# Optimization experiments

Hardware: AMD Instinct MI355X
Metric: run time of the kernel (lower is better)

## Reference

```python
import jax, jax.numpy as jnp
import numpy as np

KSIZE = 7
STRIDE = 4
SCALE = 10.0
C_IN = 64
C_INT = 16
TOP_M = 100


def _unfold(x, k, s):
    # x: [B,C,H,W] -> [B, C*k*k, L] with torch.nn.Unfold channel ordering (c, ki, kj)
    B, C, H, W = x.shape
    oh = (H - k) // s + 1
    ow = (W - k) // s + 1
    rows = jnp.arange(oh)[:, None] * s + jnp.arange(k)[None, :]  # [oh,k]
    cols = jnp.arange(ow)[:, None] * s + jnp.arange(k)[None, :]  # [ow,k]
    p = x[:, :, rows][:, :, :, :, cols]          # [B,C,oh,k,ow,k]
    p = p.transpose(0, 1, 3, 5, 2, 4)            # [B,C,k,k,oh,ow]
    return p.reshape(B, C * k * k, oh * ow)


def _fold(p, H, W, k, s):
    # inverse of _unfold with overlap-add (torch.nn.Fold semantics)
    B, D, L = p.shape
    C = D // (k * k)
    oh = (H - k) // s + 1
    ow = (W - k) // s + 1
    rows = jnp.arange(oh)[:, None] * s + jnp.arange(k)[None, :]
    cols = jnp.arange(ow)[:, None] * s + jnp.arange(k)[None, :]
    p = p.reshape(B, C, k, k, oh, ow).transpose(0, 1, 4, 2, 5, 3)  # [B,C,oh,k,ow,k]
    out = jnp.zeros((B, C, H, W), p.dtype)
    return out.at[:, :, rows[:, :, None, None], cols[None, None, :, :]].add(p)


def _conv1x1(x, w, b):
    return jnp.einsum('bchw,oc->bohw', x, w) + b[None, :, None, None]


def _conv3x3(x, w, b):
    y = jax.lax.conv_general_dilated(x, w, (1, 1), ((1, 1), (1, 1)),
                                     dimension_numbers=('NCHW', 'OIHW', 'NCHW'))
    return y + b[None, :, None, None]


def setup_inputs() -> dict:
    key = jax.random.key(0)
    ks = jax.random.split(key, 12)
    B, H, W = 4, 127, 127
    s = 0.05  # small init std keeps softmax logits in a sane range
    return {
        'x': jax.random.normal(ks[0], (B, C_IN, H, W), jnp.float32),
        'g_w': jax.random.normal(ks[1], (C_INT, C_IN, 3, 3), jnp.float32) * s,
        'g_b': jnp.zeros((C_INT,), jnp.float32),
        'theta_w': jax.random.normal(ks[2], (C_INT, C_IN), jnp.float32) * s,
        'theta_b': jnp.zeros((C_INT,), jnp.float32),
        'phi_w': jax.random.normal(ks[3], (C_INT, C_IN), jnp.float32) * s,
        'phi_b': jnp.zeros((C_INT,), jnp.float32),
        'match_w': jax.random.normal(ks[4], (C_INT, C_IN), jnp.float32) * s,
        'match_b': jnp.zeros((C_INT,), jnp.float32),
        'restore_w': jax.random.normal(ks[5], (C_IN, C_INT), jnp.float32) * s,
        'restore_b': jnp.zeros((C_IN,), jnp.float32),
    }


def reference(x, g_w, g_b, theta_w, theta_b, phi_w, phi_b,
              match_w, match_b, restore_w, restore_b):
    B, C, H, W = x.shape
    b1 = _conv3x3(x, g_w, g_b)           # [B,16,H,W]
    b2 = _conv1x1(x, theta_w, theta_b)
    b3 = _conv1x1(x, phi_w, phi_b)

    p1 = _unfold(b1, KSIZE, STRIDE).transpose(0, 2, 1)  # [B,L,D], D=16*49
    p2 = _unfold(b2, KSIZE, STRIDE).transpose(0, 2, 1)
    p3 = _unfold(b3, KSIZE, STRIDE).transpose(0, 2, 1)

    score = jnp.einsum('bld,bmd->blm', p1, p2)           # [B,L,L]
    L = score.shape[-1]
    k = min(TOP_M, L)
    vals, idx = jax.lax.top_k(score, k)                  # [B,L,k]
    bI = jnp.arange(B)[:, None, None]
    rI = jnp.arange(L)[None, :, None]
    sparse = jnp.zeros_like(score).at[bI, rI, idx].set(vals)
    attn = jax.nn.softmax(sparse * SCALE, axis=-1)

    agg = jnp.einsum('blm,bmd->bld', attn, p3).transpose(0, 2, 1)  # [B,D,L]
    out = _fold(agg, H, W, KSIZE, STRIDE)                # [B,16,H,W]

    mask = _fold(_unfold(jnp.ones_like(x), KSIZE, STRIDE), H, W, KSIZE, STRIDE)
    mask = _conv1x1(mask, match_w, match_b)              # [B,16,H,W]

    out = out / (mask + 1e-8)
    out = _conv1x1(out, restore_w, restore_b)            # [B,64,H,W]
    return out
```

## Files before the change

kernel.cpp:

```cpp
#include <hip/hip_runtime.h>
#include <hip/hip_bf16.h>

typedef __hip_bfloat16 bf16;
typedef unsigned short ushort_t;
typedef __attribute__((ext_vector_type(8))) __bf16 bfv8;
typedef __attribute__((ext_vector_type(16))) float f32x16;

#define B_   4
#define CIN  64
#define CI   16
#define H_   127
#define W_   127
#define HW   (H_*W_)
#define KS   7
#define ST   4
#define OH_  31
#define L_   961
#define D_   784
#define TOPM 100

#define N1   1032256
#define WG_O 4
#define WT_O (WG_O + 9216)
#define WP_O (WT_O + 1024)
#define BG_O (WP_O + 1024)
#define BT_O (BG_O + 16)
#define BP_O (BT_O + 16)
#define SM_O (BP_O + 16)
#define SB_O (SM_O + 16)
#define RW_O (SB_O + 16)
#define RB_O (RW_O + 1024)
#define B1_O 12448
#define S3_O (B1_O + 3*N1)
#define WB_O (S3_O + B_*D_)
#define REG_O (WB_O + 36864)
#define XHSZ 4129024
#define SROW 964
#define SCSLOT 926464
#define AGSZ 753424
#define TKROW 112
#define SLST 72
#define PKPLANE 753424
#define PKSTR   1506848
#define PADW 129
#define PADPIX (PADW*PADW)
#define XPB  (PADPIX*64)
#define XPU  ((size_t)B_ * XPB)

#define FULL_BYTES ((size_t)(REG_O + XHSZ + 4*AGSZ) * 4)
#define MID_BYTES  ((size_t)(REG_O + 4260096) * 4)

__device__ __forceinline__ float bf2f(bf16 v) { return __bfloat162float(v); }
__device__ __forceinline__ float bflo(unsigned u) { return __uint_as_float(u << 16); }
__device__ __forceinline__ float bfhi(unsigned u) { return __uint_as_float(u & 0xFFFF0000u); }

template <typename T> struct Ld;
template <> struct Ld<float> {
  static __device__ __forceinline__ float f(const void* p, int i) { return ((const float*)p)[i]; }
};
template <> struct Ld<bf16> {
  static __device__ __forceinline__ float f(const void* p, int i) { return bf2f(((const bf16*)p)[i]); }
};

__device__ __forceinline__ unsigned fmap(float f) {
  unsigned u = __float_as_uint(f);
  return (u & 0x80000000u) ? ~u : (u | 0x80000000u);
}
__device__ __forceinline__ float unfmap(unsigned kk) {
  unsigned u = (kk & 0x80000000u) ? (kk & 0x7fffffffu) : ~kk;
  return __uint_as_float(u);
}

__device__ __forceinline__ ushort_t f2bf(float x) {
  unsigned u = __float_as_uint(x);
  return (ushort_t)((u + 0x7FFFu + ((u >> 16) & 1u)) >> 16);
}
__device__ __forceinline__ void splitbf(float x, ushort_t& h, ushort_t& l) {
  h = f2bf(x);
  float hf = __uint_as_float(((unsigned)h) << 16);
  l = f2bf(x - hf);
}

__global__ void k_detect(const unsigned short* __restrict__ xh, int* __restrict__ flag) {
  int tid = threadIdx.x;
  int c = 0;
#pragma unroll
  for (int j = 0; j < 2; ++j) {
    unsigned u = xh[tid * 2 + j];
    unsigned e = (u >> 7) & 0xFF;
    if (e >= 134) c++;
  }
#pragma unroll
  for (int o = 32; o; o >>= 1) c += __shfl_down(c, o);
  if (tid == 0) *flag = (c >= 8) ? 1 : 0;
}

#define LDW(ptr, i) (f ? ((const float*)(ptr))[i] : bf2f(((const bf16*)(ptr))[i]))
__global__ __launch_bounds__(256) void k_prep(
    const int* __restrict__ flag,
    const void* g_w, const void* t_w, const void* p_w,
    const void* g_b, const void* t_b, const void* p_b,
    const void* m_w, const void* m_b, const void* r_w, const void* r_b,
    float* __restrict__ ws)
{
  int f = *flag;
  int gid = blockIdx.x * 256 + threadIdx.x;
  int gs = gridDim.x * 256;
  for (int i = gid; i < 9216; i += gs) {
    int o = i & 15, t = i >> 4, c = t & 63, tap = t >> 6;
    ws[WG_O + i] = LDW(g_w, (o * 64 + c) * 9 + tap);
  }
  for (int i = gid; i < 1024; i += gs) {
    int o = i & 15, c = i >> 4;
    ws[WT_O + i] = LDW(t_w, o * 64 + c);
    ws[WP_O + i] = LDW(p_w, o * 64 + c);
  }
  if (gid < 16) {
    ws[BG_O + gid] = LDW(g_b, gid);
    ws[BT_O + gid] = LDW(t_b, gid);
    ws[BP_O + gid] = LDW(p_b, gid);
    float s = 0.f;
    for (int c = 0; c < 64; ++c) s += LDW(m_w, gid * 64 + c);
    ws[SM_O + gid] = s;
    ws[SB_O + gid] = LDW(m_b, gid);
  }
  for (int i = gid; i < 1024; i += gs) ws[RW_O + i] = LDW(r_w, i);
  if (gid >= 64 && gid < 128) ws[RB_O + gid - 64] = LDW(r_b, gid - 64);
  ushort_t* wBh = (ushort_t*)(ws + WB_O);
  ushort_t* wBl = wBh + 9 * 64 * 64;
  for (int i = gid; i < 9 * 64 * 64; i += gs) {
    int c = i & 63, t = i >> 6, col = t & 63, tap = t >> 6;
    float v = 0.f;
    if (col < 16) v = LDW(g_w, (col * 64 + c) * 9 + tap);
    else if (col < 32) { if (tap == 4) v = LDW(t_w, (col - 16) * 64 + c); }
    else if (col < 48) { if (tap == 4) v = LDW(p_w, (col - 32) * 64 + c); }
    ushort_t h, l; splitbf(v, h, l);
    wBh[i] = h; wBl[i] = l;
  }
}

__global__ __launch_bounds__(256) void k_zpad(ushort_t* __restrict__ xhh,
                                              ushort_t* __restrict__ xhl)
{
  int idx = blockIdx.x * 256 + threadIdx.x;
  if (idx >= B_ * 512 * 8) return;
  int q = idx & 7, t = idx >> 3;
  int bp = t & 511, bb = t >> 9;
  int pp;
  if (bp < 129) pp = bp;
  else if (bp < 258) pp = 128 * PADW + (bp - 129);
  else if (bp < 385) pp = (bp - 257) * PADW;
  else pp = (bp - 384) * PADW + 128;
  size_t off = ((size_t)bb * PADPIX + pp) * 64 + q * 8;
  const int4 z = make_int4(0, 0, 0, 0);
  *(int4*)(xhh + off) = z;
  *(int4*)(xhl + off) = z;
}

__global__ __launch_bounds__(256) void k_hwc(
    const int* __restrict__ flag, const void* __restrict__ x,
    ushort_t* __restrict__ xhh, ushort_t* __restrict__ xhl)
{
  __shared__ float tile[64][65];
  int pix0 = blockIdx.x * 64;
  int tid = threadIdx.x;
  int g = tid >> 6, p = tid & 63;
  int pix = pix0 + p;
  bool ok = pix < B_ * HW;
  int bb = ok ? pix / HW : 0;
  int r  = ok ? pix - bb * HW : 0;
  if (*flag) {
    const float* xf = (const float*)x;
    for (int c = g * 16; c < g * 16 + 16; ++c)
      tile[p][c] = ok ? xf[((size_t)bb * CIN + c) * HW + r] : 0.f;
  } else {
    const bf16* xb = (const bf16*)x;
    for (int c = g * 16; c < g * 16 + 16; ++c)
      tile[p][c] = ok ? bf2f(xb[((size_t)bb * CIN + c) * HW + r]) : 0.f;
  }
  __syncthreads();
  int c2 = tid & 63, pg = tid >> 6;
  int pix2 = pix0 + pg * 16;
  int bb2 = pix2 / HW, r2 = pix2 - bb2 * HW;
  int h2 = r2 / W_, w2 = r2 - h2 * W_;
  for (int k = 0; k < 16; ++k) {
    if (pix2 + k < B_ * HW) {
      ushort_t h, l; splitbf(tile[pg * 16 + k][c2], h, l);
      size_t off = ((size_t)bb2 * PADPIX + (size_t)(h2 + 1) * PADW + (w2 + 1)) * 64 + c2;
      xhh[off] = h;
      xhl[off] = l;
    }
    if (++w2 == W_) { w2 = 0; if (++h2 == H_) { h2 = 0; ++bb2; } }
  }
}

__global__ __launch_bounds__(256) void k_conv3(
    const float* __restrict__ ws,
    const ushort_t* __restrict__ xhh, const ushort_t* __restrict__ xhl,
    ushort_t* __restrict__ b1h, ushort_t* __restrict__ b1l,
    ushort_t* __restrict__ b2h, ushort_t* __restrict__ b2l,
    ushort_t* __restrict__ b3)
{
  __shared__ ushort_t sAh[128 * SLST], sAl[128 * SLST];
  __shared__ ushort_t sBh[64 * SLST],  sBl[64 * SLST];
  int bz = blockIdx.z;
  int h = blockIdx.x;
  int tid = threadIdx.x, lane = tid & 63, wv = tid >> 6;
  int grp = lane >> 3, ch = lane & 7;

  const ushort_t* xplane = ((wv == 0) ? xhh : xhl) + (size_t)bz * XPB;
  const ushort_t* wBh_ = (const ushort_t*)(ws + WB_O);
  const ushort_t* bsrc = (wv == 2) ? wBh_ : (wBh_ + 9 * 64 * 64);
  ushort_t* dplane = (wv == 0) ? sAh : (wv == 1) ? sAl : (wv == 2) ? sBh : sBl;

  int fr = lane & 31, kh = (lane >> 5) << 3;
  int mt = (wv >> 1) << 1;
  int aoff0 = (mt * 32 + fr) * SLST + kh;
  int aoff1 = ((mt + 1) * 32 + fr) * SLST + kh;
  int boff  = (((wv & 1) << 5) + fr) * SLST + kh;

  f32x16 acc0 = {0.f,0.f,0.f,0.f,0.f,0.f,0.f,0.f,0.f,0.f,0.f,0.f,0.f,0.f,0.f,0.f};
  f32x16 acc1 = {0.f,0.f,0.f,0.f,0.f,0.f,0.f,0.f,0.f,0.f,0.f,0.f,0.f,0.f,0.f,0.f};

  int4 pv0, pv1, pv2, pv3, pv4, pv5, pv6, pv7;
  int4 pv8, pv9, pv10, pv11, pv12, pv13, pv14, pv15;

#define LC(j) pv##j = *(const int4*)(src + (j) * 512)
#define LC_A  LC(0); LC(1); LC(2); LC(3); LC(4); LC(5); LC(6); LC(7); \
              LC(8); LC(9); LC(10); LC(11); LC(12); LC(13); LC(14); LC(15)
#define LC_W  LC(0); LC(1); LC(2); LC(3); LC(4); LC(5); LC(6); LC(7)
#define WC(j) *(int4*)(d0 + (j) * 8 * SLST) = pv##j
#define WC_A  WC(0); WC(1); WC(2); WC(3); WC(4); WC(5); WC(6); WC(7); \
              WC(8); WC(9); WC(10); WC(11); WC(12); WC(13); WC(14); WC(15)
#define WC_W  WC(0); WC(1); WC(2); WC(3); WC(4); WC(5); WC(6); WC(7)

  if (wv < 2) {
    const ushort_t* src = xplane + (size_t)h * (PADW * 64) + grp * 64 + ch * 8;
    LC_A;
  } else {
    const ushort_t* src = bsrc + grp * 64 + ch * 8;
    LC_W;
  }

  for (int r = 0; r < 9; ++r) {
    __syncthreads();
    {
      ushort_t* d0 = dplane + grp * SLST + ch * 8;
      if (wv < 2) { WC_A; } else { WC_W; }
    }
    __syncthreads();
    if (r < 8) {
      int rn = r + 1;
      int dh = rn / 3 - 1, dw = rn % 3 - 1;
      if (wv < 2) {
        const ushort_t* src = xplane
            + ((size_t)(h + 1 + dh) * PADW + (1 + dw)) * 64 + grp * 64 + ch * 8;
        LC_A;
      } else {
        const ushort_t* src = bsrc + rn * 4096 + grp * 64 + ch * 8;
        LC_W;
      }
    }
#pragma unroll
    for (int t = 0; t < 4; ++t) {
      bfv8 ah0 = *(const bfv8*)(sAh + aoff0 + t * 16);
      bfv8 al0 = *(const bfv8*)(sAl + aoff0 + t * 16);
      bfv8 ah1 = *(const bfv8*)(sAh + aoff1 + t * 16);
      bfv8 al1 = *(const bfv8*)(sAl + aoff1 + t * 16);
      bfv8 bh  = *(const bfv8*)(sBh + boff + t * 16);
      bfv8 bl  = *(const bfv8*)(sBl + boff + t * 16);
      acc0 = __builtin_amdgcn_mfma_f32_32x32x16_bf16(al0, bh, acc0, 0, 0, 0);
      acc0 = __builtin_amdgcn_mfma_f32_32x32x16_bf16(ah0, bl, acc0, 0, 0, 0);
      acc0 = __builtin_amdgcn_mfma_f32_32x32x16_bf16(ah0, bh, acc0, 0, 0, 0);
      acc1 = __builtin_amdgcn_mfma_f32_32x32x16_bf16(al1, bh, acc1, 0, 0, 0);
      acc1 = __builtin_amdgcn_mfma_f32_32x32x16_bf16(ah1, bl, acc1, 0, 0, 0);
      acc1 = __builtin_amdgcn_mfma_f32_32x32x16_bf16(ah1, bh, acc1, 0, 0, 0);
    }
  }
#undef LC
#undef LC_A
#undef LC_W
#undef WC
#undef WC_A
#undef WC_W

  int nw = ((wv & 1) << 5) + fr;
#pragma unroll
  for (int s = 0; s < 2; ++s) {
    int mbase = (mt + s) * 32;
#pragma unroll
    for (int r = 0; r < 16; ++r) {
      int m = mbase + (r & 3) + ((r >> 2) << 3) + ((lane >> 5) << 2);
      if (m >= W_) continue;
      int p2 = h * W_ + m;
      size_t ob = ((size_t)bz * HW + p2) * 16;
      float val = s ? acc1[r] : acc0[r];
      if (nw < 16) {
        ushort_t h2, l2; splitbf(val + ws[BG_O + nw], h2, l2);
        b1h[ob + nw] = h2; b1l[ob + nw] = l2;
      } else if (nw < 32) {
        int o = nw - 16; ushort_t h2, l2; splitbf(val + ws[BT_O + o], h2, l2);
        b2h[ob + o] = h2; b2l[ob + o] = l2;
      } else if (nw < 48) {
        int o = nw - 32; b3[ob + o] = f2bf(val + ws[BP_O + o]);
      }
    }
  }
}

template <typename T>
__device__ __forceinline__ void convF_body(
    const void* x, const void* g_w, const void* g_b,
    const void* t_w, const void* t_b, const void* p_w, const void* p_b,
    ushort_t* b1h, ushort_t* b1l, ushort_t* b2h, ushort_t* b2l, ushort_t* b3,
    float* sgw, float* stw, float* spw)
{
  int tid = threadIdx.y * 32 + threadIdx.x;
  for (int i = tid; i < CI * CIN * 9; i += 256) sgw[i] = Ld<T>::f(g_w, i);
  for (int i = tid; i < CI * CIN; i += 256) { stw[i] = Ld<T>::f(t_w, i); spw[i] = Ld<T>::f(p_w, i); }
  __syncthreads();

  int w = blockIdx.x * 32 + threadIdx.x;
  int h = blockIdx.y * 8 + threadIdx.y;
  int b = blockIdx.z;
  if (w >= W_ || h >= H_) return;

  float a1[CI], a2[CI], a3[CI];
#pragma unroll
  for (int o = 0; o < CI; ++o) { a1[o] = 0.f; a2[o] = 0.f; a3[o] = 0.f; }

  const size_t xb = (size_t)b * CIN * HW;
  for (int c = 0; c < CIN; ++c) {
    float xv[9];
#pragma unroll
    for (int dh = 0; dh < 3; ++dh) {
      int hh = h + dh - 1;
      bool rok = ((unsigned)hh < (unsigned)H_);
#pragma unroll
      for (int dw = 0; dw < 3; ++dw) {
        int ww = w + dw - 1;
        bool ok = rok && ((unsigned)ww < (unsigned)W_);
        xv[dh * 3 + dw] = ok ? Ld<T>::f(x, (int)(xb + (size_t)c * HW + hh * W_ + ww)) : 0.f;
      }
    }
    float xc = xv[4];
#pragma unroll
    for (int o = 0; o < CI; ++o) {
      const float* gg = &sgw[(o * CIN + c) * 9];
      float s = gg[0]*xv[0] + gg[1]*xv[1] + gg[2]*xv[2]
              + gg[3]*xv[3] + gg[4]*xv[4] + gg[5]*xv[5]
              + gg[6]*xv[6] + gg[7]*xv[7] + gg[8]*xv[8];
      a1[o] += s;
      a2[o] += stw[o * CIN + c] * xc;
      a3[o] += spw[o * CIN + c] * xc;
    }
  }
  size_t base = ((size_t)b * HW + h * W_ + w) * CI;
#pragma unroll
  for (int o = 0; o < CI; ++o) {
    float v1 = a1[o] + Ld<T>::f(g_b, o);
    float v2 = a2[o] + Ld<T>::f(t_b, o);
    ushort_t hh2, ll2;
    splitbf(v1, hh2, ll2); b1h[base + o] = hh2; b1l[base + o] = ll2;
    splitbf(v2, hh2, ll2); b2h[base + o] = hh2; b2l[base + o] = ll2;
    b3[base + o] = f2bf(a3[o] + Ld<T>::f(p_b, o));
  }
}

__global__ __launch_bounds__(256) void k_convF(
    const int* __restrict__ flag, const void* x,
    const void* g_w, const void* g_b, const void* t_w, const void* t_b,
    const void* p_w, const void* p_b,
    ushort_t* __restrict__ b1h, ushort_t* __restrict__ b1l,
    ushort_t* __restrict__ b2h, ushort_t* __restrict__ b2l,
    ushort_t* __restrict__ b3)
{
  __shared__ float sgw[CI * CIN * 9];
  __shared__ float stw[CI * CIN];
  __shared__ float spw[CI * CIN];
  if (*flag) convF_body<float>(x, g_w, g_b, t_w, t_b, p_w, p_b, b1h, b1l, b2h, b2l, b3, sgw, stw, spw);
  else       convF_body<bf16 >(x, g_w, g_b, t_w, t_b, p_w, p_b, b1h, b1l, b2h, b2l, b3, sgw, stw, spw);
}

__global__ __launch_bounds__(256) void k_colsum(const ushort_t* __restrict__ b3, float* __restrict__ S3)
{
  __shared__ float red[16][17];
  int b = blockIdx.x, pos = blockIdx.y;
  int ki = pos / 7, kj = pos % 7;
  int c = threadIdx.x & 15, chunk = threadIdx.x >> 4;
  const ushort_t* B3 = b3 + (size_t)b * HW * CI;
  float s = 0.f;
  for (int l = chunk; l < L_; l += 16) {
    int lh = l / OH_, lw = l % OH_;
    s += bflo((unsigned)B3[((lh * ST + ki) * W_ + lw * ST + kj) * CI + c]);
  }
  red[chunk][c] = s;
  __syncthreads();
  if (threadIdx.x < 16) {
    float t = 0.f;
#pragma unroll
    for (int k = 0; k < 16; ++k) t += red[k][threadIdx.x];
    S3[(b * 49 + pos) * 16 + threadIdx.x] = t;
  }
}

__global__ __launch_bounds__(256) void k_pack(
    const ushort_t* __restrict__ b1h, const ushort_t* __restrict__ b1l,
    ushort_t* __restrict__ pk, int b0, unsigned pkstride_z)
{
  int idx = blockIdx.x * 256 + threadIdx.x;
  if (idx >= 961 * 98) return;
  int row = idx / 98, rem = idx - row * 98;
  int nki = rem / 14, q = rem - nki * 14;
  int slh = row / OH_, slw = row - slh * OH_;
  int src = ((slh * ST) * W_ + slw * ST + nki * W_) * 16 + q * 8;
  int dst = (nki * 961 + row) * 112 + q * 8;
  int batch = b0 + blockIdx.y;
  size_t poff = (size_t)batch * HW * CI;
  ushort_t* pkb = pk + (size_t)blockIdx.y * pkstride_z;
  *(int4*)(pkb + dst)           = *(const int4*)(b1h + poff + src);
  *(int4*)(pkb + PKPLANE + dst) = *(const int4*)(b1l + poff + src);
}

__global__ __launch_bounds__(256) void k_score(
    const ushort_t* __restrict__ b2h, const ushort_t* __restrict__ b2l,
    const ushort_t* __restrict__ pk,
    float* __restrict__ scb, int b0, unsigned scstride_z, unsigned pkstride_z)
{
  __shared__ ushort_t sAh[128 * SLST], sAl[128 * SLST];
  __shared__ ushort_t sBh[64 * SLST],  sBl[64 * SLST];
  int batch = b0 + blockIdx.z;
  size_t poff_g = (size_t)batch * HW * CI;
  float* Sc = scb + (size_t)blockIdx.z * scstride_z;

  int tid = threadIdx.x;
  int m0 = blockIdx.y * 128, n0 = blockIdx.x * 64;
  int lane = tid & 63;
  int wv = tid >> 6;
  int grp = lane >> 3, ch = lane & 7;

  const ushort_t* pkb = pk + (size_t)blockIdx.z * pkstride_z + (size_t)(wv & 1) * PKPLANE;

  int srow = n0 + lane;  if (srow > L_ - 1) srow = L_ - 1;
  int slh = srow / OH_, slw = srow - slh * OH_;
  int sbase = (slh * ST) * W_ + slw * ST;
  const ushort_t* splane = (wv == 2) ? (b2h + poff_g) : (b2l + poff_g);
  ushort_t* dplane = (wv == 0) ? sAh : (wv == 1) ? sAl : (wv == 2) ? sBh : sBl;
  ushort_t* drowB = dplane + lane * SLST;

  int fr = lane & 31;
  int kh = (lane >> 5) << 3;
  int mt = (wv >> 1) << 1;
  int aoff0 = (mt * 32 + fr) * SLST + kh;
  int aoff1 = ((mt + 1) * 32 + fr) * SLST + kh;
  int boff  = (((wv & 1) << 5) + fr) * SLST + kh;

  f32x16 acc0 = {0.f,0.f,0.f,0.f,0.f,0.f,0.f,0.f,0.f,0.f,0.f,0.f,0.f,0.f,0.f,0.f};
  f32x16 acc1 = {0.f,0.f,0.f,0.f,0.f,0.f,0.f,0.f,0.f,0.f,0.f,0.f,0.f,0.f,0.f,0.f};

  int4 pv0, pv1, pv2, pv3, pv4, pv5, pv6, pv7;
  int4 pv8, pv9, pv10, pv11, pv12, pv13, pv14, pv15;

#define LA(j) pv##j = *(const int4*)(pks + (size_t)min(m0 + 8*j + grp, 960) * 112)
#define LA_ALL LA(0); LA(1); LA(2); LA(3); LA(4); LA(5); LA(6); LA(7); \
               LA(8); LA(9); LA(10); LA(11); LA(12); LA(13); LA(14); LA(15)
#define WA(j) *(int4*)(d0 + (j) * 8 * SLST) = pv##j
#define WA_ALL WA(0); WA(1); WA(2); WA(3); WA(4); WA(5); WA(6); WA(7); \
               WA(8); WA(9); WA(10); WA(11); WA(12); WA(13); WA(14); WA(15)

  if (wv < 2) {
    const ushort_t* pks = pkb + ch * 8;
    LA_ALL;
  } else {
    const int4* s0 = (const int4*)(splane + (size_t)sbase * 16);
    pv0 = s0[0]; pv1 = s0[1]; pv2 = s0[2]; pv3 = s0[3];
    pv4 = s0[4]; pv5 = s0[5]; pv6 = s0[6]; pv7 = s0[7];
  }

  for (int r = 0; r < 14; ++r) {
    int half = r & 1;
    __syncthreads();
    if (wv < 2) {
      ushort_t* d0 = dplane + grp * SLST + ch * 8;
      if (!half) { WA_ALL; }
      else if (ch < 6) { WA_ALL; }
    } else {
      *(int4*)(drowB + 0)  = pv0;  *(int4*)(drowB + 8)  = pv1;
      *(int4*)(drowB + 16) = pv2;  *(int4*)(drowB + 24) = pv3;
      *(int4*)(drowB + 32) = pv4;  *(int4*)(drowB + 40) = pv5;
      if (!half) { *(int4*)(drowB + 48) = pv6; *(int4*)(drowB + 56) = pv7; }
    }
    __syncthreads();
    if (r < 13) {
      int rn = r + 1;
      int nki = rn >> 1, odd = rn & 1;
      if (wv < 2) {
        const ushort_t* pks = pkb + (size_t)nki * (961 * 112) + odd * 64 + ch * 8;
        if (!odd) { LA_ALL; }
        else if (ch < 6) { LA_ALL; }
      } else {
        int nkj0 = odd * 4;
        const int4* s0 = (const int4*)(splane + (size_t)(sbase + nki * W_ + nkj0) * 16);
        pv0 = s0[0]; pv1 = s0[1]; pv2 = s0[2]; pv3 = s0[3]; pv4 = s0[4]; pv5 = s0[5];
        if (!odd) { pv6 = s0[6]; pv7 = s0[7]; }
      }
    }
    if (!half) {
#pragma unroll
      for (int t = 0; t < 4; ++t) {
        bfv8 ah0 = *(const bfv8*)(sAh + aoff0 + t * 16);
        bfv8 al0 = *(const bfv8*)(sAl + aoff0 + t * 16);
        bfv8 ah1 = *(const bfv8*)(sAh + aoff1 + t * 16);
        bfv8 al1 = *(const bfv8*)(sAl + aoff1 + t * 16);
        bfv8 bh  = *(const bfv8*)(sBh + boff + t * 16);
        bfv8 bl  = *(const bfv8*)(sBl + boff + t * 16);
        acc0 = __builtin_amdgcn_mfma_f32_32x32x16_bf16(al0, bh, acc0, 0, 0, 0);
        acc0 = __builtin_amdgcn_mfma_f32_32x32x16_bf16(ah0, bl, acc0, 0, 0, 0);
        acc0 = __builtin_amdgcn_mfma_f32_32x32x16_bf16(ah0, bh, acc0, 0, 0, 0);
        acc1 = __builtin_amdgcn_mfma_f32_32x32x16_bf16(al1, bh, acc1, 0, 0, 0);
        acc1 = __builtin_amdgcn_mfma_f32_32x32x16_bf16(ah1, bl, acc1, 0, 0, 0);
        acc1 = __builtin_amdgcn_mfma_f32_32x32x16_bf16(ah1, bh, acc1, 0, 0, 0);
      }
    } else {
#pragma unroll
      for (int t = 0; t < 3; ++t) {
        bfv8 ah0 = *(const bfv8*)(sAh + aoff0 + t * 16);
        bfv8 al0 = *(const bfv8*)(sAl + aoff0 + t * 16);
        bfv8 ah1 = *(const bfv8*)(sAh + aoff1 + t * 16);
        bfv8 al1 = *(const bfv8*)(sAl + aoff1 + t * 16);
        bfv8 bh  = *(const bfv8*)(sBh + boff + t * 16);
        bfv8 bl  = *(const bfv8*)(sBl + boff + t * 16);
        acc0 = __builtin_amdgcn_mfma_f32_32x32x16_bf16(al0, bh, acc0, 0, 0, 0);
        acc0 = __builtin_amdgcn_mfma_f32_32x32x16_bf16(ah0, bl, acc0, 0, 0, 0);
        acc0 = __builtin_amdgcn_mfma_f32_32x32x16_bf16(ah0, bh, acc0, 0, 0, 0);
        acc1 = __builtin_amdgcn_mfma_f32_32x32x16_bf16(al1, bh, acc1, 0, 0, 0);
        acc1 = __builtin_amdgcn_mfma_f32_32x32x16_bf16(ah1, bl, acc1, 0, 0, 0);
        acc1 = __builtin_amdgcn_mfma_f32_32x32x16_bf16(ah1, bh, acc1, 0, 0, 0);
      }
    }
  }
#undef LA
#undef LA_ALL
#undef WA
#undef WA_ALL

  int nw = n0 + ((wv & 1) << 5) + fr;
  if (nw < L_) {
    int mw0 = m0 + mt * 32;
#pragma unroll
    for (int r = 0; r < 16; ++r) {
      int m = mw0 + (r & 3) + ((r >> 2) << 3) + ((lane >> 5) << 2);
      if (m < L_) Sc[(size_t)m * SROW + nw] = acc0[r];
    }
    int mw1 = m0 + (mt + 1) * 32;
#pragma unroll
    for (int r = 0; r < 16; ++r) {
      int m = mw1 + (r & 3) + ((r >> 2) << 3) + ((lane >> 5) << 2);
      if (m < L_) Sc[(size_t)m * SROW + nw] = acc1[r];
    }
  }
}

__global__ __launch_bounds__(256) void k_topk(
    const float* __restrict__ scb, float* __restrict__ tkw, int* __restrict__ tkp,
    unsigned scstride_z)
{
  __shared__ float swv[4][TOPM];
  __shared__ int spx[4][TOPM];
  int tid = threadIdx.x;
  int wvi = tid >> 6, lane = tid & 63;
  int l = blockIdx.x * 4 + wvi;
  if (l > L_ - 1) l = L_ - 1;
  int bz = blockIdx.y;
  const float4* row4 = (const float4*)(scb + (size_t)bz * scstride_z + (size_t)l * SROW);
  int trow = (bz * L_ + l) * TKROW;

  unsigned k[16];
#pragma unroll
  for (int q = 0; q < 4; ++q) {
    float4 v = row4[q * 64 + lane];
    int ib = (q * 64 + lane) * 4;
    k[q * 4 + 0] = (ib + 0 < L_) ? fmap(v.x) : 0u;
    k[q * 4 + 1] = (ib + 1 < L_) ? fmap(v.y) : 0u;
    k[q * 4 + 2] = (ib + 2 < L_) ? fmap(v.z) : 0u;
    k[q * 4 + 3] = (ib + 3 < L_) ? fmap(v.w) : 0u;
  }

  unsigned mk = 0;
#pragma unroll
  for (int r = 0; r < 16; ++r) mk = max(mk, k[r]);
#pragma unroll
  for (int o = 32; o; o >>= 1) mk = max(mk, (unsigned)__shfl_down((int)mk, o));
  mk = (unsigned)__shfl((int)mk, 0);
  float vmax = unfmap(mk);

  unsigned kk[16];
#pragma unroll
  for (int r = 0; r < 16; ++r) kk[r] = k[r];

  unsigned prefix = 0; int base = 0;
  for (int bit = 30; bit >= 0; bit -= 2) {
    int n3 = 0, n2 = 0, n1 = 0;
#pragma unroll
    for (int r = 0; r < 16; ++r) {
      unsigned f = (kk[r] >> bit) & 3u;
      n3 += (int)__popcll(__ballot(f == 3u));
      n2 += (int)__popcll(__ballot(f >= 2u));
      n1 += (int)__popcll(__ballot(f >= 1u));
    }
    unsigned ch;
    if (base + n3 >= TOPM) ch = 3;
    else if (base + n2 >= TOPM) { ch = 2; base += n3; }
    else if (base + n1 >= TOPM) { ch = 1; base += n2; }
    else { ch = 0; base += n1; }
    prefix |= ch << bit;
#pragma unroll
    for (int r = 0; r < 16; ++r) {
      unsigned f = (kk[r] >> bit) & 3u;
      kk[r] = (f == ch) ? kk[r] : 0u;
    }
  }
  int nA = base;
  int needT = TOPM - nA;

  int cA = 0, cT = 0;
#pragma unroll
  for (int r = 0; r < 16; ++r) { cA += (k[r] > prefix); cT += (k[r] == prefix); }
  int pk = cA | (cT << 16);
  int incl = pk;
#pragma unroll
  for (int o = 1; o < 64; o <<= 1) { int t = __shfl_up(incl, o); if (lane >= o) incl += t; }
  int excl = incl - pk;
  int tA = excl & 0xFFFF, tT = excl >> 16;

  float M = fmaxf(10.f * vmax, 0.f);
  float e0 = __expf(-M);
  float z = 0.f;
#pragma unroll
  for (int r = 0; r < 16; ++r) {
    unsigned kr = k[r];
    int slot = -1;
    if (kr > prefix) slot = tA++;
    else if (kr == prefix) { if (tT < needT) slot = nA + tT; tT++; }
    if (slot >= 0) {
      float v = unfmap(kr);
      float wv = __expf(10.f * v - M);
      swv[wvi][slot] = wv; z += wv;
      int gi = 256 * (r >> 2) + 4 * lane + (r & 3);
      int lh = gi / OH_, lw = gi - lh * OH_;
      spx[wvi][slot] = ((lh * ST) * W_ + lw * ST) * CI;
    }
  }
#pragma unroll
  for (int o = 32; o; o >>= 1) z += __shfl_down(z, o);
  z = __shfl(z, 0);
  float Z = z + (float)(L_ - TOPM) * e0;
  float invZ = 1.f / Z;
  float w0 = e0 / Z;
  __syncthreads();
#pragma unroll
  for (int s0 = 0; s0 < 2; ++s0) {
    int s = lane + 64 * s0;
    if (s < TOPM) {
      tkw[trow + s] = swv[wvi][s] * invZ - w0;
      tkp[trow + s] = spx[wvi][s];
    }
  }
  if (lane == 0) tkw[trow + TOPM] = w0;
}

__global__ __launch_bounds__(128) void k_pv(
    const float* __restrict__ tkw, const int* __restrict__ tkp,
    const ushort_t* __restrict__ b3, const float* __restrict__ s3,
    float* __restrict__ agb, int b0, unsigned agstride_z)
{
  int l = blockIdx.x, bz = blockIdx.y;
  int batch = b0 + bz;
  int trow = (bz * L_ + l) * TKROW;
  const ushort_t* B3 = b3 + (size_t)batch * HW * CI;
  const float* S3 = s3 + (size_t)batch * D_;
  float* agg = agb + (size_t)bz * agstride_z;
  int tid = threadIdx.x;
  if (tid >= 98) return;

  float w0 = tkw[trow + TOPM];
  int pos = tid >> 1;
  int c0 = (tid & 1) << 3;
  int ki = pos / 7, kj = pos - (pos / 7) * 7;
  int poff = (ki * W_ + kj) * CI + c0;

  float a0 = 0.f, a1 = 0.f, a2 = 0.f, a3 = 0.f;
  float a4 = 0.f, a5 = 0.f, a6 = 0.f, a7 = 0.f;
  for (int j0 = 0; j0 < TOPM; j0 += 4) {
    float w_0 = tkw[trow + j0 + 0];
    float w_1 = tkw[trow + j0 + 1];
    float w_2 = tkw[trow + j0 + 2];
    float w_3 = tkw[trow + j0 + 3];
    int p_0 = tkp[trow + j0 + 0];
    int p_1 = tkp[trow + j0 + 1];
    int p_2 = tkp[trow + j0 + 2];
    int p_3 = tkp[trow + j0 + 3];
    const uint4 q0 = *(const uint4*)(B3 + p_0 + poff);
    const uint4 q1 = *(const uint4*)(B3 + p_1 + poff);
    const uint4 q2 = *(const uint4*)(B3 + p_2 + poff);
    const uint4 q3 = *(const uint4*)(B3 + p_3 + poff);
    a0 += w_0 * bflo(q0.x); a1 += w_0 * bfhi(q0.x); a2 += w_0 * bflo(q0.y); a3 += w_0 * bfhi(q0.y);
    a4 += w_0 * bflo(q0.z); a5 += w_0 * bfhi(q0.z); a6 += w_0 * bflo(q0.w); a7 += w_0 * bfhi(q0.w);
    a0 += w_1 * bflo(q1.x); a1 += w_1 * bfhi(q1.x); a2 += w_1 * bflo(q1.y); a3 += w_1 * bfhi(q1.y);
    a4 += w_1 * bflo(q1.z); a5 += w_1 * bfhi(q1.z); a6 += w_1 * bflo(q1.w); a7 += w_1 * bfhi(q1.w);
    a0 += w_2 * bflo(q2.x); a1 += w_2 * bfhi(q2.x); a2 += w_2 * bflo(q2.y); a3 += w_2 * bfhi(q2.y);
    a4 += w_2 * bflo(q2.z); a5 += w_2 * bfhi(q2.z); a6 += w_2 * bflo(q2.w); a7 += w_2 * bfhi(q2.w);
    a0 += w_3 * bflo(q3.x); a1 += w_3 * bfhi(q3.x); a2 += w_3 * bflo(q3.y); a3 += w_3 * bfhi(q3.y);
    a4 += w_3 * bflo(q3.z); a5 += w_3 * bfhi(q3.z); a6 += w_3 * bflo(q3.w); a7 += w_3 * bfhi(q3.w);
  }
  const float4 s40 = *(const float4*)(S3 + tid * 8);
  const float4 s41 = *(const float4*)(S3 + tid * 8 + 4);
  a0 += w0 * s40.x; a1 += w0 * s40.y; a2 += w0 * s40.z; a3 += w0 * s40.w;
  a4 += w0 * s41.x; a5 += w0 * s41.y; a6 += w0 * s41.z; a7 += w0 * s41.w;
  float* dst = agg + (size_t)l * D_ + tid * 8;
  *(float4*)(dst)     = make_float4(a0, a1, a2, a3);
  *(float4*)(dst + 4) = make_float4(a4, a5, a6, a7);
}

__global__ __launch_bounds__(256) void k_fold(
    const int* __restrict__ flag, const float* __restrict__ ws,
    const float* __restrict__ agb, void* __restrict__ out,
    int b0, unsigned agstride_z)
{
  __shared__ float srw[CIN * CI];
  int tid = threadIdx.x;
  for (int i = tid; i < CIN * CI; i += 256) srw[i] = ws[RW_O + i];
  __syncthreads();

  int bz = blockIdx.y;
  int batch = b0 + bz;
  const float* agg = agb + (size_t)bz * agstride_z;

  int gid = blockIdx.x * 256 + tid;
  if (gid >= HW) return;
  int h = gid / W_;
  int w = gid % W_;

  int lh0 = (h >= KS - 1) ? ((h - (KS - 1) + (ST - 1)) >> 2) : 0;
  int lh1 = min(OH_ - 1, h >> 2);
  int lw0 = (w >= KS - 1) ? ((w - (KS - 1) + (ST - 1)) >> 2) : 0;
  int lw1 = min(OH_ - 1, w >> 2);

  float t[CI];
#pragma unroll
  for (int c = 0; c < CI; ++c) t[c] = 0.f;
  for (int lh = lh0; lh <= lh1; ++lh) {
    int ki = h - ST * lh;
    for (int lw = lw0; lw <= lw1; ++lw) {
      int kj = w - ST * lw;
      const float* pb = agg + (size_t)(lh * OH_ + lw) * D_ + (ki * KS + kj) * CI;
      float4 q0 = *(const float4*)(pb);
      float4 q1 = *(const float4*)(pb + 4);
      float4 q2 = *(const float4*)(pb + 8);
      float4 q3 = *(const float4*)(pb + 12);
      t[0] += q0.x; t[1] += q0.y; t[2] += q0.z; t[3] += q0.w;
      t[4] += q1.x; t[5] += q1.y; t[6] += q1.z; t[7] += q1.w;
      t[8] += q2.x; t[9] += q2.y; t[10] += q2.z; t[11] += q2.w;
      t[12] += q3.x; t[13] += q3.y; t[14] += q3.z; t[15] += q3.w;
    }
  }
  float cnt = (float)((lh1 - lh0 + 1) * (lw1 - lw0 + 1));
  float r[CI];
#pragma unroll
  for (int c = 0; c < CI; ++c) r[c] = t[c] / (cnt * ws[SM_O + c] + ws[SB_O + c] + 1e-8f);

  size_t ob = (size_t)batch * CIN * HW + (size_t)h * W_ + w;
  if (*flag) {
    float* of = (float*)out;
#pragma unroll
    for (int o = 0; o < CIN; ++o) {
      float s = ws[RB_O + o];
#pragma unroll
      for (int c = 0; c < CI; ++c) s += srw[o * CI + c] * r[c];
      of[ob + (size_t)o * HW] = s;
    }
  } else {
    bf16* of = (bf16*)out;
#pragma unroll
    for (int o = 0; o < CIN; ++o) {
      float s = ws[RB_O + o];
#pragma unroll
      for (int c = 0; c < CI; ++c) s += srw[o * CI + c] * r[c];
      of[ob + (size_t)o * HW] = __float2bfloat16(s);
    }
  }
}

extern "C" void kernel_launch(void* const* d_in, const int* in_sizes, int n_in,
                              void* d_out, int out_size, void* d_ws, size_t ws_size,
                              hipStream_t stream)
{
  const void* x    = d_in[0];
  const void* g_w  = d_in[1];
  const void* g_b  = d_in[2];
  const void* th_w = d_in[3];
  const void* th_b = d_in[4];
  const void* ph_w = d_in[5];
  const void* ph_b = d_in[6];
  const void* m_w  = d_in[7];
  const void* m_b  = d_in[8];
  const void* r_w  = d_in[9];
  const void* r_b  = d_in[10];

  float* W = (float*)d_ws;
  int* flag = (int*)d_ws;
  ushort_t* planes = (ushort_t*)(W + B1_O);
  ushort_t* b1h = planes;
  ushort_t* b1l = planes + (size_t)N1;
  ushort_t* b2h = planes + (size_t)2 * N1;
  ushort_t* b2l = planes + (size_t)3 * N1;
  ushort_t* b3  = planes + (size_t)4 * N1;
  float* s3 = W + S3_O;

  k_detect<<<1, 64, 0, stream>>>((const unsigned short*)x, flag);
  k_prep<<<64, 256, 0, stream>>>(flag, g_w, th_w, ph_w, g_b, th_b, ph_b,
                                 m_w, m_b, r_w, r_b, W);

  if (ws_size >= FULL_BYTES) {
    ushort_t* xhh = (ushort_t*)(W + REG_O);
    ushort_t* xhl = xhh + XPU;
    float* sc = W + REG_O;
    float* ag = W + REG_O + XHSZ;
    ushort_t* pk = (ushort_t*)ag;
    float* tkw = W + B1_O + N1;
    int*   tkp = (int*)(W + B1_O + N1 + N1 / 2);
    k_zpad<<<64, 256, 0, stream>>>(xhh, xhl);
    k_hwc<<<dim3((B_ * HW + 63) / 64), 256, 0, stream>>>(flag, x, xhh, xhl);
    k_conv3<<<dim3(H_, 1, B_), 256, 0, stream>>>(
        W, xhh, xhl, b1h, b1l, b2h, b2l, b3);
    k_pack<<<dim3(368, B_), 256, 0, stream>>>(b1h, b1l, pk, 0, PKSTR);
    k_colsum<<<dim3(B_, 49), 256, 0, stream>>>(b3, s3);
    k_score<<<dim3(16, 8, B_), 256, 0, stream>>>(b2h, b2l, pk, sc, 0, SCSLOT, PKSTR);
    k_topk<<<dim3((L_ + 3) / 4, B_), 256, 0, stream>>>(sc, tkw, tkp, SCSLOT);
    k_pv<<<dim3(L_, B_), 128, 0, stream>>>(tkw, tkp, b3, s3, ag, 0, AGSZ);
    k_fold<<<dim3(64, B_), 256, 0, stream>>>(flag, W, ag, d_out, 0, AGSZ);
  } else if (ws_size >= MID_BYTES) {
    ushort_t* xhh = (ushort_t*)(W + REG_O);
    ushort_t* xhl = xhh + XPU;
    float* sc = W + REG_O;
    float* ag = W + REG_O + SCSLOT;
    ushort_t* pk = (ushort_t*)ag;
    k_zpad<<<64, 256, 0, stream>>>(xhh, xhl);
    k_hwc<<<dim3((B_ * HW + 63) / 64), 256, 0, stream>>>(flag, x, xhh, xhl);
    k_conv3<<<dim3(H_, 1, B_), 256, 0, stream>>>(
        W, xhh, xhl, b1h, b1l, b2h, b2l, b3);
    k_colsum<<<dim3(B_, 49), 256, 0, stream>>>(b3, s3);
    for (int b = 0; b < B_; ++b) {
      float* tkw = W + B1_O + N1 + (size_t)b * (HW * CI / 2);
      int*   tkp = (int*)(W + B1_O + N1 + N1 / 2 + (size_t)b * (HW * CI / 2));
      k_pack<<<dim3(368, 1), 256, 0, stream>>>(b1h, b1l, pk, b, 0);
      k_score<<<dim3(16, 8, 1), 256, 0, stream>>>(b2h, b2l, pk, sc, b, 0, 0);
      k_topk<<<dim3((L_ + 3) / 4, 1), 256, 0, stream>>>(sc, tkw, tkp, 0);
      k_pv<<<dim3(L_, 1), 128, 0, stream>>>(tkw, tkp, b3, s3, ag, b, 0);
      k_fold<<<dim3(64, 1), 256, 0, stream>>>(flag, W, ag, d_out, b, 0);
    }
  } else {
    float* sc = W + REG_O;
    float* ag = W + REG_O + SCSLOT;
    ushort_t* pk = (ushort_t*)ag;
    k_convF<<<dim3(4, 16, B_), dim3(32, 8, 1), 0, stream>>>(
        flag, x, g_w, g_b, th_w, th_b, ph_w, ph_b, b1h, b1l, b2h, b2l, b3);
    k_colsum<<<dim3(B_, 49), 256, 0, stream>>>(b3, s3);
    for (int b = 0; b < B_; ++b) {
      float* tkw = W + B1_O + N1 + (size_t)b * (HW * CI / 2);
      int*   tkp = (int*)(W + B1_O + N1 + N1 / 2 + (size_t)b * (HW * CI / 2));
      k_pack<<<dim3(368, 1), 256, 0, stream>>>(b1h, b1l, pk, b, 0);
      k_score<<<dim3(16, 8, 1), 256, 0, stream>>>(b2h, b2l, pk, sc, b, 0, 0);
      k_topk<<<dim3((L_ + 3) / 4, 1), 256, 0, stream>>>(sc, tkw, tkp, 0);
      k_pv<<<dim3(L_, 1), 128, 0, stream>>>(tkw, tkp, b3, s3, ag, b, 0);
      k_fold<<<dim3(64, 1), 256, 0, stream>>>(flag, W, ag, d_out, b, 0);
    }
  }
}
```

Baseline: 262.8 us.

## Fuse detect and zero-pad into prep, and pack b1 patches inside conv3

Folds the dtype-detect kernel and the zero-padding kernel into k_prep, so each block computes the flag and writes it to the workspace. In the full-workspace path, k_conv3 now stages its b1 output rows in shared memory and writes the packed unfold layout straight to the pk buffer, which removes the separate k_pack launch and the b1 global round trip. This saves several launches and one memory pass. The cost is extra shared-memory traffic and barriers in conv3, a new workspace layout, and every block redundantly reading x to compute the flag.

```diff
diff --git a/kernel.cpp b/kernel.cpp
--- a/kernel.cpp
+++ b/kernel.cpp
@@ -34,7 +34,6 @@
 #define S3_O (B1_O + 3*N1)
 #define WB_O (S3_O + B_*D_)
 #define REG_O (WB_O + 36864)
-#define XHSZ 4129024
 #define SROW 964
 #define SCSLOT 926464
 #define AGSZ 753424
@@ -46,9 +45,11 @@
 #define PADPIX (PADW*PADW)
 #define XPB  (PADPIX*64)
 #define XPU  ((size_t)B_ * XPB)
-
-#define FULL_BYTES ((size_t)(REG_O + XHSZ + 4*AGSZ) * 4)
-#define MID_BYTES  ((size_t)(REG_O + 4260096) * 4)
+#define PLANES_FL 4260096
+#define PK_O (REG_O + PLANES_FL)
+
+#define FULL_BYTES ((size_t)(PK_O + 3013696) * 4)
+#define MID_BYTES  ((size_t)(REG_O + PLANES_FL) * 4)
 
 __device__ __forceinline__ float bf2f(bf16 v) { return __bfloat162float(v); }
 __device__ __forceinline__ float bflo(unsigned u) { return __uint_as_float(u << 16); }
@@ -81,29 +82,35 @@
   l = f2bf(x - hf);
 }
 
-__global__ void k_detect(const unsigned short* __restrict__ xh, int* __restrict__ flag) {
-  int tid = threadIdx.x;
-  int c = 0;
-#pragma unroll
-  for (int j = 0; j < 2; ++j) {
-    unsigned u = xh[tid * 2 + j];
-    unsigned e = (u >> 7) & 0xFF;
-    if (e >= 134) c++;
-  }
-#pragma unroll
-  for (int o = 32; o; o >>= 1) c += __shfl_down(c, o);
-  if (tid == 0) *flag = (c >= 8) ? 1 : 0;
-}
-
 #define LDW(ptr, i) (f ? ((const float*)(ptr))[i] : bf2f(((const bf16*)(ptr))[i]))
 __global__ __launch_bounds__(256) void k_prep(
-    const int* __restrict__ flag,
+    const void* __restrict__ x,
     const void* g_w, const void* t_w, const void* p_w,
     const void* g_b, const void* t_b, const void* p_b,
     const void* m_w, const void* m_b, const void* r_w, const void* r_b,
-    float* __restrict__ ws)
-{
-  int f = *flag;
+    float* __restrict__ ws,
+    ushort_t* __restrict__ xhh, ushort_t* __restrict__ xhl)
+{
+  __shared__ int sflag;
+  {
+    const unsigned short* xh = (const unsigned short*)x;
+    if (threadIdx.x < 64) {
+      int c = 0;
+#pragma unroll
+      for (int j = 0; j < 2; ++j) {
+        unsigned u = xh[threadIdx.x * 2 + j];
+        unsigned e = (u >> 7) & 0xFF;
+        if (e >= 134) c++;
+      }
+#pragma unroll
+      for (int o = 32; o; o >>= 1) c += __shfl_down(c, o);
+      if (threadIdx.x == 0) sflag = (c >= 8) ? 1 : 0;
+    }
+  }
+  __syncthreads();
+  int f = sflag;
+  if (blockIdx.x == 0 && threadIdx.x == 0) *(int*)ws = f;
+
   int gid = blockIdx.x * 256 + threadIdx.x;
   int gs = gridDim.x * 256;
   for (int i = gid; i < 9216; i += gs) {
@@ -137,24 +144,21 @@
     ushort_t h, l; splitbf(v, h, l);
     wBh[i] = h; wBl[i] = l;
   }
-}
-
-__global__ __launch_bounds__(256) void k_zpad(ushort_t* __restrict__ xhh,
-                                              ushort_t* __restrict__ xhl)
-{
-  int idx = blockIdx.x * 256 + threadIdx.x;
-  if (idx >= B_ * 512 * 8) return;
-  int q = idx & 7, t = idx >> 3;
-  int bp = t & 511, bb = t >> 9;
-  int pp;
-  if (bp < 129) pp = bp;
-  else if (bp < 258) pp = 128 * PADW + (bp - 129);
-  else if (bp < 385) pp = (bp - 257) * PADW;
-  else pp = (bp - 384) * PADW + 128;
-  size_t off = ((size_t)bb * PADPIX + pp) * 64 + q * 8;
-  const int4 z = make_int4(0, 0, 0, 0);
-  *(int4*)(xhh + off) = z;
-  *(int4*)(xhl + off) = z;
+  if (xhh) {
+    const int4 z = make_int4(0, 0, 0, 0);
+    for (int idx = gid; idx < B_ * 512 * 8; idx += gs) {
+      int q = idx & 7, t = idx >> 3;
+      int bp = t & 511, bb = t >> 9;
+      int pp;
+      if (bp < 129) pp = bp;
+      else if (bp < 258) pp = 128 * PADW + (bp - 129);
+      else if (bp < 385) pp = (bp - 257) * PADW;
+      else pp = (bp - 384) * PADW + 128;
+      size_t off = ((size_t)bb * PADPIX + pp) * 64 + q * 8;
+      *(int4*)(xhh + off) = z;
+      *(int4*)(xhl + off) = z;
+    }
+  }
 }
 
 __global__ __launch_bounds__(256) void k_hwc(
@@ -199,7 +203,7 @@
     const ushort_t* __restrict__ xhh, const ushort_t* __restrict__ xhl,
     ushort_t* __restrict__ b1h, ushort_t* __restrict__ b1l,
     ushort_t* __restrict__ b2h, ushort_t* __restrict__ b2l,
-    ushort_t* __restrict__ b3)
+    ushort_t* __restrict__ b3, ushort_t* __restrict__ pk)
 {
   __shared__ ushort_t sAh[128 * SLST], sAl[128 * SLST];
   __shared__ ushort_t sBh[64 * SLST],  sBl[64 * SLST];
@@ -285,24 +289,68 @@
 #undef WC_W
 
   int nw = ((wv & 1) << 5) + fr;
-#pragma unroll
-  for (int s = 0; s < 2; ++s) {
-    int mbase = (mt + s) * 32;
-#pragma unroll
-    for (int r = 0; r < 16; ++r) {
-      int m = mbase + (r & 3) + ((r >> 2) << 3) + ((lane >> 5) << 2);
-      if (m >= W_) continue;
-      int p2 = h * W_ + m;
-      size_t ob = ((size_t)bz * HW + p2) * 16;
-      float val = s ? acc1[r] : acc0[r];
-      if (nw < 16) {
-        ushort_t h2, l2; splitbf(val + ws[BG_O + nw], h2, l2);
-        b1h[ob + nw] = h2; b1l[ob + nw] = l2;
-      } else if (nw < 32) {
-        int o = nw - 16; ushort_t h2, l2; splitbf(val + ws[BT_O + o], h2, l2);
-        b2h[ob + o] = h2; b2l[ob + o] = l2;
-      } else if (nw < 48) {
-        int o = nw - 32; b3[ob + o] = f2bf(val + ws[BP_O + o]);
+  if (pk) {
+    __syncthreads();
+    ushort_t* sb1h = sAh;
+    ushort_t* sb1l = sAl;
+#pragma unroll
+    for (int s = 0; s < 2; ++s) {
+      int mbase = (mt + s) * 32;
+#pragma unroll
+      for (int r = 0; r < 16; ++r) {
+        int m = mbase + (r & 3) + ((r >> 2) << 3) + ((lane >> 5) << 2);
+        float val = s ? acc1[r] : acc0[r];
+        if (nw < 16) {
+          ushort_t h2, l2; splitbf(val + ws[BG_O + nw], h2, l2);
+          sb1h[m * 16 + nw] = h2; sb1l[m * 16 + nw] = l2;
+        } else if (m < W_) {
+          size_t ob = ((size_t)bz * HW + h * W_ + m) * 16;
+          if (nw < 32) {
+            int o = nw - 16; ushort_t h2, l2; splitbf(val + ws[BT_O + o], h2, l2);
+            b2h[ob + o] = h2; b2l[ob + o] = l2;
+          } else if (nw < 48) {
+            int o = nw - 32; b3[ob + o] = f2bf(val + ws[BP_O + o]);
+          }
+        }
+      }
+    }
+    __syncthreads();
+    ushort_t* pkb = pk + (size_t)bz * PKSTR;
+    int slh_lo = (h >= 6) ? ((h - 3) >> 2) : 0;
+    int slh_hi = h >> 2; if (slh_hi > 30) slh_hi = 30;
+    for (int slh = slh_lo; slh <= slh_hi; ++slh) {
+      int nki = h - 4 * slh;
+      size_t rb = ((size_t)nki * 961 + slh * 31) * 112;
+      for (int t = tid; t < 31 * 14; t += 256) {
+        int slw = t / 14, q = t - slw * 14;
+        int m = slw * 4 + (q >> 1);
+        int c0 = (q & 1) << 3;
+        int4 vh = *(int4*)(sb1h + m * 16 + c0);
+        int4 vl = *(int4*)(sb1l + m * 16 + c0);
+        size_t doff = rb + (size_t)slw * 112 + q * 8;
+        *(int4*)(pkb + doff)           = vh;
+        *(int4*)(pkb + PKPLANE + doff) = vl;
+      }
+    }
+  } else {
+#pragma unroll
+    for (int s = 0; s < 2; ++s) {
+      int mbase = (mt + s) * 32;
+#pragma unroll
+      for (int r = 0; r < 16; ++r) {
+        int m = mbase + (r & 3) + ((r >> 2) << 3) + ((lane >> 5) << 2);
+        if (m >= W_) continue;
+        size_t ob = ((size_t)bz * HW + h * W_ + m) * 16;
+        float val = s ? acc1[r] : acc0[r];
+        if (nw < 16) {
+          ushort_t h2, l2; splitbf(val + ws[BG_O + nw], h2, l2);
+          b1h[ob + nw] = h2; b1l[ob + nw] = l2;
+        } else if (nw < 32) {
+          int o = nw - 16; ushort_t h2, l2; splitbf(val + ws[BT_O + o], h2, l2);
+          b2h[ob + o] = h2; b2l[ob + o] = l2;
+        } else if (nw < 48) {
+          int o = nw - 32; b3[ob + o] = f2bf(val + ws[BP_O + o]);
+        }
       }
     }
   }
@@ -817,23 +865,19 @@
   ushort_t* b3  = planes + (size_t)4 * N1;
   float* s3 = W + S3_O;
 
-  k_detect<<<1, 64, 0, stream>>>((const unsigned short*)x, flag);
-  k_prep<<<64, 256, 0, stream>>>(flag, g_w, th_w, ph_w, g_b, th_b, ph_b,
-                                 m_w, m_b, r_w, r_b, W);
-
   if (ws_size >= FULL_BYTES) {
     ushort_t* xhh = (ushort_t*)(W + REG_O);
     ushort_t* xhl = xhh + XPU;
     float* sc = W + REG_O;
-    float* ag = W + REG_O + XHSZ;
-    ushort_t* pk = (ushort_t*)ag;
+    ushort_t* pk = (ushort_t*)(W + PK_O);
+    float* ag = W + PK_O;
     float* tkw = W + B1_O + N1;
     int*   tkp = (int*)(W + B1_O + N1 + N1 / 2);
-    k_zpad<<<64, 256, 0, stream>>>(xhh, xhl);
+    k_prep<<<64, 256, 0, stream>>>(x, g_w, th_w, ph_w, g_b, th_b, ph_b,
+                                   m_w, m_b, r_w, r_b, W, xhh, xhl);
     k_hwc<<<dim3((B_ * HW + 63) / 64), 256, 0, stream>>>(flag, x, xhh, xhl);
     k_conv3<<<dim3(H_, 1, B_), 256, 0, stream>>>(
-        W, xhh, xhl, b1h, b1l, b2h, b2l, b3);
-    k_pack<<<dim3(368, B_), 256, 0, stream>>>(b1h, b1l, pk, 0, PKSTR);
+        W, xhh, xhl, b1h, b1l, b2h, b2l, b3, pk);
     k_colsum<<<dim3(B_, 49), 256, 0, stream>>>(b3, s3);
     k_score<<<dim3(16, 8, B_), 256, 0, stream>>>(b2h, b2l, pk, sc, 0, SCSLOT, PKSTR);
     k_topk<<<dim3((L_ + 3) / 4, B_), 256, 0, stream>>>(sc, tkw, tkp, SCSLOT);
@@ -845,10 +889,11 @@
     float* sc = W + REG_O;
     float* ag = W + REG_O + SCSLOT;
     ushort_t* pk = (ushort_t*)ag;
-    k_zpad<<<64, 256, 0, stream>>>(xhh, xhl);
+    k_prep<<<64, 256, 0, stream>>>(x, g_w, th_w, ph_w, g_b, th_b, ph_b,
+                                   m_w, m_b, r_w, r_b, W, xhh, xhl);
     k_hwc<<<dim3((B_ * HW + 63) / 64), 256, 0, stream>>>(flag, x, xhh, xhl);
     k_conv3<<<dim3(H_, 1, B_), 256, 0, stream>>>(
-        W, xhh, xhl, b1h, b1l, b2h, b2l, b3);
+        W, xhh, xhl, b1h, b1l, b2h, b2l, b3, (ushort_t*)nullptr);
     k_colsum<<<dim3(B_, 49), 256, 0, stream>>>(b3, s3);
     for (int b = 0; b < B_; ++b) {
       float* tkw = W + B1_O + N1 + (size_t)b * (HW * CI / 2);
@@ -863,6 +908,9 @@
     float* sc = W + REG_O;
     float* ag = W + REG_O + SCSLOT;
     ushort_t* pk = (ushort_t*)ag;
+    k_prep<<<64, 256, 0, stream>>>(x, g_w, th_w, ph_w, g_b, th_b, ph_b,
+                                   m_w, m_b, r_w, r_b, W,
+                                   (ushort_t*)nullptr, (ushort_t*)nullptr);
     k_convF<<<dim3(4, 16, B_), dim3(32, 8, 1), 0, stream>>>(
         flag, x, g_w, g_b, th_w, th_b, ph_w, ph_b, b1h, b1l, b2h, b2l, b3);
     k_colsum<<<dim3(B_, 49), 256, 0, stream>>>(b3, s3);
```

Result: faster. 255.6 us (-2.7%).
